# Performance work log

Measured on AMD Instinct MI355X. Metric: run time of the kernel, lower is better.

The kernel has to match this reference:

```python
import jax, jax.numpy as jnp
import numpy as np

N_NODES = 100_000
N_EDGES = 2_500_000
HID = 32
SE3_NORM = 1.0 / np.sqrt(32.0)  # e3nn path normalization for 32x0e -> 32x0e


def setup_inputs() -> dict:
    key = jax.random.key(0)
    ks = jax.random.split(key, 14)
    inp = {
        "pos": jax.random.normal(ks[0], (N_NODES, 3), dtype=jnp.float32),
        "edge_index": jax.random.randint(ks[1], (2, N_EDGES), 0, N_NODES, dtype=jnp.int64),
        "Wl1": jax.random.normal(ks[2], (2, HID), dtype=jnp.float32) * 0.5,
        "bl1": jax.random.normal(ks[3], (HID,), dtype=jnp.float32) * 0.1,
        "Wr1": jax.random.normal(ks[4], (2, HID), dtype=jnp.float32) * 0.5,
        "Wl2": jax.random.normal(ks[5], (HID, HID), dtype=jnp.float32) * 0.15,
        "bl2": jax.random.normal(ks[6], (HID,), dtype=jnp.float32) * 0.1,
        "Wr2": jax.random.normal(ks[7], (HID, HID), dtype=jnp.float32) * 0.15,
        "Wse1": jax.random.normal(ks[8], (HID, HID), dtype=jnp.float32) * 0.15,
        "Wse2": jax.random.normal(ks[9], (HID, HID), dtype=jnp.float32) * 0.15,
        "W3": jax.random.normal(ks[10], (HID, HID), dtype=jnp.float32) * 0.15,
        "b3": jax.random.normal(ks[11], (HID,), dtype=jnp.float32) * 0.1,
        "W4": jax.random.normal(ks[12], (HID, 1), dtype=jnp.float32) * 0.15,
        "b4": jax.random.normal(ks[13], (1,), dtype=jnp.float32) * 0.1,
        "alpha": jnp.float32(0.5),
    }
    return inp


def _sage_conv(x, src, dst, Wl, bl, Wr, n_nodes):
    # gather messages from source nodes, scatter-sum onto destination nodes
    agg = jax.ops.segment_sum(x[src], dst, num_segments=n_nodes)  # [N, d_in]
    return agg @ Wl + bl + x @ Wr  # lin_l(agg) + lin_r(x); lin_r has no bias


def reference(pos, edge_index, Wl1, bl1, Wr1, Wl2, bl2, Wr2, Wse1, Wse2, W3, b3, W4, b4, alpha):
    n = pos.shape[0]
    x = pos[:, :2]                       # [N, 2]
    src, dst = edge_index[0], edge_index[1]

    h1 = _sage_conv(x, src, dst, Wl1, bl1, Wr1, n)   # [N, 32]
    h1 = jax.nn.leaky_relu(h1, negative_slope=0.01)  # dropout = identity (eval)
    h1 = (h1 @ Wse1) * SE3_NORM                      # SE3Linear 32x0e->32x0e

    h2 = _sage_conv(h1, src, dst, Wl2, bl2, Wr2, n)
    h2 = jax.nn.leaky_relu(h2, negative_slope=0.01)
    h2 = (h2 @ Wse2) * SE3_NORM

    x_skip = alpha * h1 + h2
    x_out = jax.nn.relu(x_skip @ W3 + b3)            # mlp3 (dropout identity)
    pred = x_out @ W4 + b4                           # mlp4
    return pred.squeeze(-1)                          # [N]
```

## Files before the change

### kernel.cpp

```cpp
#include <hip/hip_runtime.h>
#include <hip/hip_fp16.h>

#define HID 32
#define LEAKY 0.01f
#define SE3NORM 0.17677669529663687f
#define SCAN_TILE 1024
#define NBK 128
#define GA 256


__global__ void k_bhist(const int* __restrict__ ei, int* __restrict__ bh,
                        int E, int B1, int chunk) {
    extern __shared__ int lh[];
    int g = blockIdx.x;
    for (int i = threadIdx.x; i < B1; i += 256) lh[i] = 0;
    __syncthreads();
    int beg = g * chunk, end = min(E, beg + chunk);
    for (int e = beg + (int)threadIdx.x; e < end; e += 256)
        atomicAdd(&lh[ei[E + e] >> 7], 1);
    __syncthreads();
    for (int b = threadIdx.x; b < B1; b += 256) bh[b * GA + g] = lh[b];
}

__global__ void k_scan1(int* __restrict__ data, int* __restrict__ bsum, int M) {
    __shared__ int lds[256];
    int t = threadIdx.x;
    int base = blockIdx.x * SCAN_TILE + t * 4;
    int v0 = (base + 0 < M) ? data[base + 0] : 0;
    int v1 = (base + 1 < M) ? data[base + 1] : 0;
    int v2 = (base + 2 < M) ? data[base + 2] : 0;
    int v3 = (base + 3 < M) ? data[base + 3] : 0;
    int s = v0 + v1 + v2 + v3;
    lds[t] = s;
    __syncthreads();
    for (int off = 1; off < 256; off <<= 1) {
        int x = (t >= off) ? lds[t - off] : 0;
        __syncthreads();
        lds[t] += x;
        __syncthreads();
    }
    int ex = lds[t] - s;
    if (base + 0 < M) data[base + 0] = ex;
    if (base + 1 < M) data[base + 1] = ex + v0;
    if (base + 2 < M) data[base + 2] = ex + v0 + v1;
    if (base + 3 < M) data[base + 3] = ex + v0 + v1 + v2;
    if (t == 255) bsum[blockIdx.x] = lds[255];
}

__global__ void k_scan2(int* __restrict__ bsum, int B) {
    __shared__ int lds[256];
    int t = threadIdx.x;
    int v = (t < B) ? bsum[t] : 0;
    lds[t] = v;
    __syncthreads();
    for (int off = 1; off < 256; off <<= 1) {
        int x = (t >= off) ? lds[t - off] : 0;
        __syncthreads();
        lds[t] += x;
        __syncthreads();
    }
    if (t < B) bsum[t] = lds[t] - v;
}

__global__ void k_scan3(int* __restrict__ data, const int* __restrict__ bsum,
                        int* __restrict__ cursor, int M, int N) {
    int i = blockIdx.x * blockDim.x + threadIdx.x;
    if (i >= M) return;
    int off = data[i] + bsum[i / SCAN_TILE];
    data[i] = off;
    if (cursor && i < N) cursor[i] = off;
}

__global__ void k_bscatter(const int* __restrict__ ei, const int* __restrict__ bh,
                           int* __restrict__ bucketed, int E, int B1, int chunk) {
    extern __shared__ int cur[];
    int g = blockIdx.x;
    for (int b = threadIdx.x; b < B1; b += 256) cur[b] = bh[b * GA + g];
    __syncthreads();
    int beg = g * chunk, end = min(E, beg + chunk);
    for (int e = beg + (int)threadIdx.x; e < end; e += 256) {
        int d = ei[E + e];
        int s = ei[e];
        int b = d >> 7;
        int p = atomicAdd(&cur[b], 1);
        bucketed[p] = s | ((d & (NBK - 1)) << 24);
    }
}

__global__ void k_bsort(const int* __restrict__ bh, const int* __restrict__ bucketed,
                        int* __restrict__ sorted_src, int* __restrict__ offsets,
                        int E, int N, int B1) {
    __shared__ int hist[NBK], sc[NBK], base[NBK];
    int b = blockIdx.x;
    int t = threadIdx.x;
    int bs = bh[b * GA];
    int be = (b == B1 - 1) ? E : bh[(b + 1) * GA];
    if (t < NBK) hist[t] = 0;
    __syncthreads();
    for (int e = bs + t; e < be; e += 256)
        atomicAdd(&hist[bucketed[e] >> 24], 1);
    __syncthreads();
    int v = (t < NBK) ? hist[t] : 0;
    if (t < NBK) sc[t] = v;
    __syncthreads();
    for (int off = 1; off < NBK; off <<= 1) {
        int x = (t < NBK && t >= off) ? sc[t - off] : 0;
        __syncthreads();
        if (t < NBK) sc[t] += x;
        __syncthreads();
    }
    if (t < NBK) base[t] = sc[t] - v;
    __syncthreads();
    if (t < NBK) hist[t] = base[t];
    __syncthreads();
    for (int e = bs + t; e < be; e += 256) {
        int pv = bucketed[e];
        int p = atomicAdd(&hist[pv >> 24], 1);
        sorted_src[bs + p] = pv & 0x00FFFFFF;
    }
    int node = b * NBK + t;
    if (t < NBK && node < N) offsets[node] = bs + base[t];
    if (b == B1 - 1 && t == 0) offsets[N] = E;
}

__global__ void k_hist_rank(const int* __restrict__ ei, int* __restrict__ hist,
                            int* __restrict__ rank, int E) {
    int base = (blockIdx.x * blockDim.x + threadIdx.x) * 4;
#pragma unroll
    for (int u = 0; u < 4; u++) {
        int e = base + u;
        if (e < E) rank[e] = atomicAdd(&hist[ei[E + e]], 1);
    }
}
__global__ void k_hist(const int* __restrict__ ei, int* __restrict__ hist, int E) {
    int base = (blockIdx.x * blockDim.x + threadIdx.x) * 4;
#pragma unroll
    for (int u = 0; u < 4; u++) {
        int e = base + u;
        if (e < E) atomicAdd(&hist[ei[E + e]], 1);
    }
}
__global__ void k_scatter_rank(const int* __restrict__ ei, const int* __restrict__ offsets,
                               const int* __restrict__ rank, int* __restrict__ sorted_src, int E) {
    int base = (blockIdx.x * blockDim.x + threadIdx.x) * 4;
#pragma unroll
    for (int u = 0; u < 4; u++) {
        int e = base + u;
        if (e < E) sorted_src[offsets[ei[E + e]] + rank[e]] = ei[e];
    }
}
__global__ void k_scatter_atomic(const int* __restrict__ ei, int* __restrict__ cursor,
                                 int* __restrict__ sorted_src, int E) {
    int base = (blockIdx.x * blockDim.x + threadIdx.x) * 4;
#pragma unroll
    for (int u = 0; u < 4; u++) {
        int e = base + u;
        if (e < E) {
            int p = atomicAdd(&cursor[ei[E + e]], 1);
            sorted_src[p] = ei[e];
        }
    }
}

__global__ void k_node1(const int* __restrict__ offsets, const int* __restrict__ sorted_src,
                        const float* __restrict__ pos,
                        const float* __restrict__ Wl1, const float* __restrict__ bl1,
                        const float* __restrict__ Wr1, const float* __restrict__ Wse1,
                        __half* __restrict__ h1out, int N) {
    __shared__ float sWl1[2 * HID], sWr1[2 * HID], sbl1[HID], sWse1[HID * HID];
    for (int i = threadIdx.x; i < 2 * HID; i += blockDim.x) { sWl1[i] = Wl1[i]; sWr1[i] = Wr1[i]; }
    for (int i = threadIdx.x; i < HID; i += blockDim.x) sbl1[i] = bl1[i];
    for (int i = threadIdx.x; i < HID * HID; i += blockDim.x) sWse1[i] = Wse1[i];
    __syncthreads();
    int i = blockIdx.x * blockDim.x + threadIdx.x;
    if (i >= N) return;
    int beg = offsets[i], end = offsets[i + 1];
    float a0 = 0.f, a1 = 0.f;
    int e = beg;
    for (; e + 4 <= end; e += 4) {
        int s0 = sorted_src[e], s1 = sorted_src[e + 1], s2 = sorted_src[e + 2], s3 = sorted_src[e + 3];
        a0 += pos[s0 * 3] + pos[s1 * 3] + pos[s2 * 3] + pos[s3 * 3];
        a1 += pos[s0 * 3 + 1] + pos[s1 * 3 + 1] + pos[s2 * 3 + 1] + pos[s3 * 3 + 1];
    }
    for (; e < end; e++) {
        int s = sorted_src[e];
        a0 += pos[s * 3];
        a1 += pos[s * 3 + 1];
    }
    float x0 = pos[3 * i], x1 = pos[3 * i + 1];
    float h[HID];
#pragma unroll
    for (int j = 0; j < HID; j++) {
        float v = a0 * sWl1[j] + a1 * sWl1[HID + j] + sbl1[j] + x0 * sWr1[j] + x1 * sWr1[HID + j];
        h[j] = v > 0.f ? v : LEAKY * v;
    }
    union Pack8 { __half h[8]; float4 v; };
#pragma unroll
    for (int c = 0; c < HID / 8; c++) {
        Pack8 p;
#pragma unroll
        for (int jj = 0; jj < 8; jj++) {
            int j = c * 8 + jj;
            float acc = 0.f;
#pragma unroll
            for (int k = 0; k < HID; k++) acc += h[k] * sWse1[k * HID + j];
            p.h[jj] = __float2half(acc * SE3NORM);
        }
        *(float4*)&h1out[(size_t)i * HID + c * 8] = p.v;
    }
}

__global__ void k_node2out(const int* __restrict__ offsets, const int* __restrict__ sorted_src,
                           const __half* __restrict__ h1,
                           const float* __restrict__ Wl2, const float* __restrict__ bl2,
                           const float* __restrict__ Wr2, const float* __restrict__ Wse2,
                           const float* __restrict__ W3, const float* __restrict__ b3,
                           const float* __restrict__ W4, const float* __restrict__ b4,
                           const float* __restrict__ alpha_p,
                           float* __restrict__ out, int N) {
    __shared__ float sWl2[HID * HID], sWr2[HID * HID], sWse2[HID * HID], sW3[HID * HID];
    __shared__ float sbl2[HID], sb3[HID], sW4[HID];
    __shared__ float sb4, salpha;
    __shared__ float sA[32][HID + 1], sB[32][HID + 1];
    for (int i = threadIdx.x; i < HID * HID; i += blockDim.x) {
        sWl2[i] = Wl2[i]; sWr2[i] = Wr2[i]; sWse2[i] = Wse2[i]; sW3[i] = W3[i];
    }
    for (int i = threadIdx.x; i < HID; i += blockDim.x) { sbl2[i] = bl2[i]; sb3[i] = b3[i]; sW4[i] = W4[i]; }
    if (threadIdx.x == 0) { sb4 = b4[0]; salpha = alpha_p[0]; }
    __syncthreads();

    const int lt = threadIdx.x;
    const int nodeL = lt >> 3;
    const int t = lt & 7;
    const int node = blockIdx.x * 32 + nodeL;
    const bool live = node < N;

    float hvr[4];
    if (live) {
        int beg = offsets[node], end = offsets[node + 1];
        float4 acc = make_float4(0.f, 0.f, 0.f, 0.f);
        int e = beg;
        for (; e + 4 <= end; e += 4) {
            int s0 = sorted_src[e], s1 = sorted_src[e + 1];
            int s2 = sorted_src[e + 2], s3 = sorted_src[e + 3];
            float2 r0 = *(const float2*)&h1[(size_t)s0 * HID + t * 4];
            float2 r1 = *(const float2*)&h1[(size_t)s1 * HID + t * 4];
            float2 r2 = *(const float2*)&h1[(size_t)s2 * HID + t * 4];
            float2 r3 = *(const float2*)&h1[(size_t)s3 * HID + t * 4];
            const float2* rs[4] = {&r0, &r1, &r2, &r3};
#pragma unroll
            for (int u = 0; u < 4; u++) {
                __half2 p01 = *(const __half2*)&rs[u]->x;
                __half2 p23 = *(const __half2*)&rs[u]->y;
                acc.x += __low2float(p01); acc.y += __high2float(p01);
                acc.z += __low2float(p23); acc.w += __high2float(p23);
            }
        }
        for (; e < end; e++) {
            int s = sorted_src[e];
            float2 r = *(const float2*)&h1[(size_t)s * HID + t * 4];
            __half2 p01 = *(const __half2*)&r.x;
            __half2 p23 = *(const __half2*)&r.y;
            acc.x += __low2float(p01); acc.y += __high2float(p01);
            acc.z += __low2float(p23); acc.w += __high2float(p23);
        }
        float2 ro = *(const float2*)&h1[(size_t)node * HID + t * 4];
        __half2 o01 = *(const __half2*)&ro.x;
        __half2 o23 = *(const __half2*)&ro.y;
        hvr[0] = __low2float(o01); hvr[1] = __high2float(o01);
        hvr[2] = __low2float(o23); hvr[3] = __high2float(o23);
        sA[nodeL][t * 4 + 0] = acc.x; sA[nodeL][t * 4 + 1] = acc.y;
        sA[nodeL][t * 4 + 2] = acc.z; sA[nodeL][t * 4 + 3] = acc.w;
        sB[nodeL][t * 4 + 0] = hvr[0]; sB[nodeL][t * 4 + 1] = hvr[1];
        sB[nodeL][t * 4 + 2] = hvr[2]; sB[nodeL][t * 4 + 3] = hvr[3];
    }
    __syncthreads();

    float h2r[4];
    if (live) {
#pragma unroll
        for (int jj = 0; jj < 4; jj++) {
            int j = t * 4 + jj;
            float acc = sbl2[j];
#pragma unroll
            for (int k = 0; k < HID; k++)
                acc += sA[nodeL][k] * sWl2[k * HID + j] + sB[nodeL][k] * sWr2[k * HID + j];
            h2r[jj] = acc > 0.f ? acc : LEAKY * acc;
        }
    }
    __syncthreads();
    if (live) {
#pragma unroll
        for (int jj = 0; jj < 4; jj++) sA[nodeL][t * 4 + jj] = h2r[jj];
    }
    __syncthreads();

    if (live) {
#pragma unroll
        for (int jj = 0; jj < 4; jj++) {
            int j = t * 4 + jj;
            float acc = 0.f;
#pragma unroll
            for (int k = 0; k < HID; k++) acc += sA[nodeL][k] * sWse2[k * HID + j];
            sB[nodeL][j] = salpha * hvr[jj] + acc * SE3NORM;
        }
    }
    __syncthreads();

    float part = 0.f;
#pragma unroll
    for (int jj = 0; jj < 4; jj++) {
        int j = t * 4 + jj;
        float acc = sb3[j];
        if (live) {
#pragma unroll
            for (int k = 0; k < HID; k++) acc += sB[nodeL][k] * sW3[k * HID + j];
        }
        part += (acc > 0.f ? acc : 0.f) * sW4[j];
    }
    part += __shfl_xor(part, 1);
    part += __shfl_xor(part, 2);
    part += __shfl_xor(part, 4);
    if (live && t == 0) out[node] = part + sb4;
}

extern "C" void kernel_launch(void* const* d_in, const int* in_sizes, int n_in,
                              void* d_out, int out_size, void* d_ws, size_t ws_size,
                              hipStream_t stream) {
    const float* pos  = (const float*)d_in[0];
    const int*   ei   = (const int*)d_in[1];
    const float* Wl1  = (const float*)d_in[2];
    const float* bl1  = (const float*)d_in[3];
    const float* Wr1  = (const float*)d_in[4];
    const float* Wl2  = (const float*)d_in[5];
    const float* bl2  = (const float*)d_in[6];
    const float* Wr2  = (const float*)d_in[7];
    const float* Wse1 = (const float*)d_in[8];
    const float* Wse2 = (const float*)d_in[9];
    const float* W3   = (const float*)d_in[10];
    const float* b3   = (const float*)d_in[11];
    const float* W4   = (const float*)d_in[12];
    const float* b4   = (const float*)d_in[13];
    const float* alp  = (const float*)d_in[14];
    float* out = (float*)d_out;

    const int N = in_sizes[0] / 3;
    const int E = in_sizes[1] / 2;
    const int blk = 256;
    const size_t h1bytes = (size_t)N * HID * sizeof(__half);

    const int B1 = (N + NBK - 1) / NBK;
    const int M2 = B1 * GA;
    const int S2 = (M2 + SCAN_TILE - 1) / SCAN_TILE;
    {
        int* bh         = (int*)d_ws;
        int* bsum       = bh + M2;
        int* bucketed   = bsum + 256;
        int* sorted_src = bucketed + E;
        int* offsets    = sorted_src + E;
        uintptr_t hp = ((uintptr_t)(offsets + N + 1) + 15) & ~(uintptr_t)15;
        size_t need = (hp - (uintptr_t)d_ws) + h1bytes;
        if (need <= ws_size && S2 <= 256) {
            __half* h1 = (__half*)hp;
            const int chunk = (E + GA - 1) / GA;
            const size_t ldsB = (size_t)B1 * sizeof(int);
            k_bhist<<<GA, 256, ldsB, stream>>>(ei, bh, E, B1, chunk);
            k_scan1<<<S2, 256, 0, stream>>>(bh, bsum, M2);
            k_scan2<<<1, 256, 0, stream>>>(bsum, S2);
            k_scan3<<<(M2 + blk - 1) / blk, blk, 0, stream>>>(bh, bsum, nullptr, M2, 0);
            k_bscatter<<<GA, 256, ldsB, stream>>>(ei, bh, bucketed, E, B1, chunk);
            k_bsort<<<B1, 256, 0, stream>>>(bh, bucketed, sorted_src, offsets, E, N, B1);
            k_node1<<<(N + blk - 1) / blk, blk, 0, stream>>>(offsets, sorted_src, pos,
                                                             Wl1, bl1, Wr1, Wse1, h1, N);
            k_node2out<<<(N + 31) / 32, 256, 0, stream>>>(offsets, sorted_src, h1,
                                                          Wl2, bl2, Wr2, Wse2,
                                                          W3, b3, W4, b4, alp, out, N);
            return;
        }
    }

    const int M = N + 1;
    const int B = (M + SCAN_TILE - 1) / SCAN_TILE;
    int* hist       = (int*)d_ws;
    int* offsets    = hist + M;
    int* bsum       = offsets + M;
    int* sorted_src = bsum + 256;
    int* aux        = sorted_src + E;
    uintptr_t hpA = ((uintptr_t)(aux + E) + 15) & ~(uintptr_t)15;
    uintptr_t hpB = ((uintptr_t)(aux + N) + 15) & ~(uintptr_t)15;
    size_t needA = (hpA - (uintptr_t)d_ws) + h1bytes;
    const bool useRank = (needA <= ws_size);
    __half* h1 = (__half*)(useRank ? hpA : hpB);

    hipMemsetAsync(hist, 0, (size_t)M * sizeof(int), stream);
    const int egrid4 = (E / 4 + blk) / blk;
    if (useRank) {
        k_hist_rank<<<egrid4, blk, 0, stream>>>(ei, hist, aux, E);
    } else {
        k_hist<<<egrid4, blk, 0, stream>>>(ei, hist, E);
    }
    k_scan1<<<B, 256, 0, stream>>>(hist, bsum, M);
    k_scan2<<<1, 256, 0, stream>>>(bsum, B);
    k_scan3<<<(M + blk - 1) / blk, blk, 0, stream>>>(hist, bsum, useRank ? nullptr : aux, M, N);
    int* offs = hist;
    if (useRank) {
        k_scatter_rank<<<egrid4, blk, 0, stream>>>(ei, offs, aux, sorted_src, E);
    } else {
        k_scatter_atomic<<<egrid4, blk, 0, stream>>>(ei, aux, sorted_src, E);
    }
    k_node1<<<(N + blk - 1) / blk, blk, 0, stream>>>(offs, sorted_src, pos, Wl1, bl1, Wr1, Wse1, h1, N);
    k_node2out<<<(N + 31) / 32, 256, 0, stream>>>(offs, sorted_src, h1, Wl2, bl2, Wr2, Wse2,
                                                  W3, b3, W4, b4, alp, out, N);
}
```

Baseline: 288.8 us.

## Partition edges by source range to localize layer-2 gathers in cache

Edges are bucketed by source-node range (4 ranges) as well as destination block. Layer-2 aggregation then runs as four passes, each gathering h1 rows from only a quarter of the nodes so the working set fits in cache, and accumulates into an fp32 agg2 buffer. A separate head kernel does the dense MLP afterwards. The price is extra passes over agg2 (read-modify-write on each pass), more bucket bins and scan work, and extra kernel launches. GA is also halved and the fallback path is simplified.

```diff
diff --git a/kernel.cpp b/kernel.cpp
--- a/kernel.cpp
+++ b/kernel.cpp
@@ -6,20 +6,29 @@
 #define SE3NORM 0.17677669529663687f
 #define SCAN_TILE 1024
 #define NBK 128
-#define GA 256
-
+#define GA 128
+#define RR 4
+
+
+__device__ __forceinline__ int src_range(int s, unsigned magic) {
+    int r = (int)__umulhi((unsigned)s, magic);
+    return r < RR - 1 ? r : RR - 1;
+}
 
 __global__ void k_bhist(const int* __restrict__ ei, int* __restrict__ bh,
-                        int E, int B1, int chunk) {
+                        int E, int B1, int B2, int chunk, unsigned magic) {
     extern __shared__ int lh[];
     int g = blockIdx.x;
-    for (int i = threadIdx.x; i < B1; i += 256) lh[i] = 0;
+    for (int i = threadIdx.x; i < B2; i += 256) lh[i] = 0;
     __syncthreads();
     int beg = g * chunk, end = min(E, beg + chunk);
-    for (int e = beg + (int)threadIdx.x; e < end; e += 256)
-        atomicAdd(&lh[ei[E + e] >> 7], 1);
-    __syncthreads();
-    for (int b = threadIdx.x; b < B1; b += 256) bh[b * GA + g] = lh[b];
+    for (int e = beg + (int)threadIdx.x; e < end; e += 256) {
+        int s = ei[e];
+        int d = ei[E + e];
+        atomicAdd(&lh[src_range(s, magic) * B1 + (d >> 7)], 1);
+    }
+    __syncthreads();
+    for (int b = threadIdx.x; b < B2; b += 256) bh[b * GA + g] = lh[b];
 }
 
 __global__ void k_scan1(int* __restrict__ data, int* __restrict__ bsum, int M) {
@@ -50,8 +59,13 @@
 __global__ void k_scan2(int* __restrict__ bsum, int B) {
     __shared__ int lds[256];
     int t = threadIdx.x;
-    int v = (t < B) ? bsum[t] : 0;
-    lds[t] = v;
+    int base = t * 4;
+    int v0 = (base + 0 < B) ? bsum[base + 0] : 0;
+    int v1 = (base + 1 < B) ? bsum[base + 1] : 0;
+    int v2 = (base + 2 < B) ? bsum[base + 2] : 0;
+    int v3 = (base + 3 < B) ? bsum[base + 3] : 0;
+    int s = v0 + v1 + v2 + v3;
+    lds[t] = s;
     __syncthreads();
     for (int off = 1; off < 256; off <<= 1) {
         int x = (t >= off) ? lds[t - off] : 0;
@@ -59,7 +73,11 @@
         lds[t] += x;
         __syncthreads();
     }
-    if (t < B) bsum[t] = lds[t] - v;
+    int ex = lds[t] - s;
+    if (base + 0 < B) bsum[base + 0] = ex;
+    if (base + 1 < B) bsum[base + 1] = ex + v0;
+    if (base + 2 < B) bsum[base + 2] = ex + v0 + v1;
+    if (base + 3 < B) bsum[base + 3] = ex + v0 + v1 + v2;
 }
 
 __global__ void k_scan3(int* __restrict__ data, const int* __restrict__ bsum,
@@ -72,16 +90,17 @@
 }
 
 __global__ void k_bscatter(const int* __restrict__ ei, const int* __restrict__ bh,
-                           int* __restrict__ bucketed, int E, int B1, int chunk) {
+                           int* __restrict__ bucketed, int E, int B1, int B2,
+                           int chunk, unsigned magic) {
     extern __shared__ int cur[];
     int g = blockIdx.x;
-    for (int b = threadIdx.x; b < B1; b += 256) cur[b] = bh[b * GA + g];
+    for (int b = threadIdx.x; b < B2; b += 256) cur[b] = bh[b * GA + g];
     __syncthreads();
     int beg = g * chunk, end = min(E, beg + chunk);
     for (int e = beg + (int)threadIdx.x; e < end; e += 256) {
+        int s = ei[e];
         int d = ei[E + e];
-        int s = ei[e];
-        int b = d >> 7;
+        int b = src_range(s, magic) * B1 + (d >> 7);
         int p = atomicAdd(&cur[b], 1);
         bucketed[p] = s | ((d & (NBK - 1)) << 24);
     }
@@ -89,12 +108,14 @@
 
 __global__ void k_bsort(const int* __restrict__ bh, const int* __restrict__ bucketed,
                         int* __restrict__ sorted_src, int* __restrict__ offsets,
-                        int E, int N, int B1) {
+                        int E, int N, int B1, int B2) {
     __shared__ int hist[NBK], sc[NBK], base[NBK];
-    int b = blockIdx.x;
+    int b2 = blockIdx.x;
+    int r  = b2 / B1;
+    int cb = b2 - r * B1;
     int t = threadIdx.x;
-    int bs = bh[b * GA];
-    int be = (b == B1 - 1) ? E : bh[(b + 1) * GA];
+    int bs = bh[b2 * GA];
+    int be = (b2 == B2 - 1) ? E : bh[(b2 + 1) * GA];
     if (t < NBK) hist[t] = 0;
     __syncthreads();
     for (int e = bs + t; e < be; e += 256)
@@ -118,9 +139,9 @@
         int p = atomicAdd(&hist[pv >> 24], 1);
         sorted_src[bs + p] = pv & 0x00FFFFFF;
     }
-    int node = b * NBK + t;
-    if (t < NBK && node < N) offsets[node] = bs + base[t];
-    if (b == B1 - 1 && t == 0) offsets[N] = E;
+    int node = cb * NBK + t;
+    if (t < NBK && node < N) offsets[(size_t)r * N + node] = bs + base[t];
+    if (b2 == B2 - 1 && t == 0) offsets[(size_t)RR * N] = E;
 }
 
 __global__ void k_hist_rank(const int* __restrict__ ei, int* __restrict__ hist,
@@ -132,14 +153,6 @@
         if (e < E) rank[e] = atomicAdd(&hist[ei[E + e]], 1);
     }
 }
-__global__ void k_hist(const int* __restrict__ ei, int* __restrict__ hist, int E) {
-    int base = (blockIdx.x * blockDim.x + threadIdx.x) * 4;
-#pragma unroll
-    for (int u = 0; u < 4; u++) {
-        int e = base + u;
-        if (e < E) atomicAdd(&hist[ei[E + e]], 1);
-    }
-}
 __global__ void k_scatter_rank(const int* __restrict__ ei, const int* __restrict__ offsets,
                                const int* __restrict__ rank, int* __restrict__ sorted_src, int E) {
     int base = (blockIdx.x * blockDim.x + threadIdx.x) * 4;
@@ -147,18 +160,6 @@
     for (int u = 0; u < 4; u++) {
         int e = base + u;
         if (e < E) sorted_src[offsets[ei[E + e]] + rank[e]] = ei[e];
-    }
-}
-__global__ void k_scatter_atomic(const int* __restrict__ ei, int* __restrict__ cursor,
-                                 int* __restrict__ sorted_src, int E) {
-    int base = (blockIdx.x * blockDim.x + threadIdx.x) * 4;
-#pragma unroll
-    for (int u = 0; u < 4; u++) {
-        int e = base + u;
-        if (e < E) {
-            int p = atomicAdd(&cursor[ei[E + e]], 1);
-            sorted_src[p] = ei[e];
-        }
     }
 }
 
@@ -166,7 +167,7 @@
                         const float* __restrict__ pos,
                         const float* __restrict__ Wl1, const float* __restrict__ bl1,
                         const float* __restrict__ Wr1, const float* __restrict__ Wse1,
-                        __half* __restrict__ h1out, int N) {
+                        __half* __restrict__ h1out, int N, int Rr) {
     __shared__ float sWl1[2 * HID], sWr1[2 * HID], sbl1[HID], sWse1[HID * HID];
     for (int i = threadIdx.x; i < 2 * HID; i += blockDim.x) { sWl1[i] = Wl1[i]; sWr1[i] = Wr1[i]; }
     for (int i = threadIdx.x; i < HID; i += blockDim.x) sbl1[i] = bl1[i];
@@ -174,18 +175,20 @@
     __syncthreads();
     int i = blockIdx.x * blockDim.x + threadIdx.x;
     if (i >= N) return;
-    int beg = offsets[i], end = offsets[i + 1];
     float a0 = 0.f, a1 = 0.f;
-    int e = beg;
-    for (; e + 4 <= end; e += 4) {
-        int s0 = sorted_src[e], s1 = sorted_src[e + 1], s2 = sorted_src[e + 2], s3 = sorted_src[e + 3];
-        a0 += pos[s0 * 3] + pos[s1 * 3] + pos[s2 * 3] + pos[s3 * 3];
-        a1 += pos[s0 * 3 + 1] + pos[s1 * 3 + 1] + pos[s2 * 3 + 1] + pos[s3 * 3 + 1];
-    }
-    for (; e < end; e++) {
-        int s = sorted_src[e];
-        a0 += pos[s * 3];
-        a1 += pos[s * 3 + 1];
+    for (int r = 0; r < Rr; r++) {
+        int beg = offsets[(size_t)r * N + i], end = offsets[(size_t)r * N + i + 1];
+        int e = beg;
+        for (; e + 4 <= end; e += 4) {
+            int s0 = sorted_src[e], s1 = sorted_src[e + 1], s2 = sorted_src[e + 2], s3 = sorted_src[e + 3];
+            a0 += pos[s0 * 3] + pos[s1 * 3] + pos[s2 * 3] + pos[s3 * 3];
+            a1 += pos[s0 * 3 + 1] + pos[s1 * 3 + 1] + pos[s2 * 3 + 1] + pos[s3 * 3 + 1];
+        }
+        for (; e < end; e++) {
+            int s = sorted_src[e];
+            a0 += pos[s * 3];
+            a1 += pos[s * 3 + 1];
+        }
     }
     float x0 = pos[3 * i], x1 = pos[3 * i + 1];
     float h[HID];
@@ -208,6 +211,132 @@
         }
         *(float4*)&h1out[(size_t)i * HID + c * 8] = p.v;
     }
+}
+
+__global__ void k_node2agg(const int* __restrict__ offsets, const int* __restrict__ sorted_src,
+                           const __half* __restrict__ h1, float* __restrict__ agg2,
+                           int N, int r) {
+    int lt = blockIdx.x * blockDim.x + threadIdx.x;
+    int node = lt >> 3;
+    int t = lt & 7;
+    if (node >= N) return;
+    int beg = offsets[(size_t)r * N + node], end = offsets[(size_t)r * N + node + 1];
+    float4 acc;
+    if (r == 0) acc = make_float4(0.f, 0.f, 0.f, 0.f);
+    else        acc = *(const float4*)&agg2[(size_t)node * HID + t * 4];
+    int e = beg;
+    for (; e + 4 <= end; e += 4) {
+        int s0 = sorted_src[e], s1 = sorted_src[e + 1];
+        int s2 = sorted_src[e + 2], s3 = sorted_src[e + 3];
+        float2 r0 = *(const float2*)&h1[(size_t)s0 * HID + t * 4];
+        float2 r1 = *(const float2*)&h1[(size_t)s1 * HID + t * 4];
+        float2 r2 = *(const float2*)&h1[(size_t)s2 * HID + t * 4];
+        float2 r3 = *(const float2*)&h1[(size_t)s3 * HID + t * 4];
+        const float2* rs[4] = {&r0, &r1, &r2, &r3};
+#pragma unroll
+        for (int u = 0; u < 4; u++) {
+            __half2 p01 = *(const __half2*)&rs[u]->x;
+            __half2 p23 = *(const __half2*)&rs[u]->y;
+            acc.x += __low2float(p01); acc.y += __high2float(p01);
+            acc.z += __low2float(p23); acc.w += __high2float(p23);
+        }
+    }
+    for (; e < end; e++) {
+        int s = sorted_src[e];
+        float2 rr = *(const float2*)&h1[(size_t)s * HID + t * 4];
+        __half2 p01 = *(const __half2*)&rr.x;
+        __half2 p23 = *(const __half2*)&rr.y;
+        acc.x += __low2float(p01); acc.y += __high2float(p01);
+        acc.z += __low2float(p23); acc.w += __high2float(p23);
+    }
+    *(float4*)&agg2[(size_t)node * HID + t * 4] = acc;
+}
+
+__global__ void k_node2head(const float* __restrict__ agg2, const __half* __restrict__ h1,
+                            const float* __restrict__ Wl2, const float* __restrict__ bl2,
+                            const float* __restrict__ Wr2, const float* __restrict__ Wse2,
+                            const float* __restrict__ W3, const float* __restrict__ b3,
+                            const float* __restrict__ W4, const float* __restrict__ b4,
+                            const float* __restrict__ alpha_p,
+                            float* __restrict__ out, int N) {
+    __shared__ float sWl2[HID * HID], sWr2[HID * HID], sWse2[HID * HID], sW3[HID * HID];
+    __shared__ float sbl2[HID], sb3[HID], sW4[HID];
+    __shared__ float sb4, salpha;
+    __shared__ float sA[32][HID + 1], sB[32][HID + 1];
+    for (int i = threadIdx.x; i < HID * HID; i += blockDim.x) {
+        sWl2[i] = Wl2[i]; sWr2[i] = Wr2[i]; sWse2[i] = Wse2[i]; sW3[i] = W3[i];
+    }
+    for (int i = threadIdx.x; i < HID; i += blockDim.x) { sbl2[i] = bl2[i]; sb3[i] = b3[i]; sW4[i] = W4[i]; }
+    if (threadIdx.x == 0) { sb4 = b4[0]; salpha = alpha_p[0]; }
+    __syncthreads();
+
+    const int lt = threadIdx.x;
+    const int nodeL = lt >> 3;
+    const int t = lt & 7;
+    const int node = blockIdx.x * 32 + nodeL;
+    const bool live = node < N;
+
+    float hvr[4];
+    if (live) {
+        float4 a = *(const float4*)&agg2[(size_t)node * HID + t * 4];
+        float2 ro = *(const float2*)&h1[(size_t)node * HID + t * 4];
+        __half2 o01 = *(const __half2*)&ro.x;
+        __half2 o23 = *(const __half2*)&ro.y;
+        hvr[0] = __low2float(o01); hvr[1] = __high2float(o01);
+        hvr[2] = __low2float(o23); hvr[3] = __high2float(o23);
+        sA[nodeL][t * 4 + 0] = a.x; sA[nodeL][t * 4 + 1] = a.y;
+        sA[nodeL][t * 4 + 2] = a.z; sA[nodeL][t * 4 + 3] = a.w;
+        sB[nodeL][t * 4 + 0] = hvr[0]; sB[nodeL][t * 4 + 1] = hvr[1];
+        sB[nodeL][t * 4 + 2] = hvr[2]; sB[nodeL][t * 4 + 3] = hvr[3];
+    }
+    __syncthreads();
+
+    float h2r[4];
+    if (live) {
+#pragma unroll
+        for (int jj = 0; jj < 4; jj++) {
+            int j = t * 4 + jj;
+            float acc = sbl2[j];
+#pragma unroll
+            for (int k = 0; k < HID; k++)
+                acc += sA[nodeL][k] * sWl2[k * HID + j] + sB[nodeL][k] * sWr2[k * HID + j];
+            h2r[jj] = acc > 0.f ? acc : LEAKY * acc;
+        }
+    }
+    __syncthreads();
+    if (live) {
+#pragma unroll
+        for (int jj = 0; jj < 4; jj++) sA[nodeL][t * 4 + jj] = h2r[jj];
+    }
+    __syncthreads();
+
+    if (live) {
+#pragma unroll
+        for (int jj = 0; jj < 4; jj++) {
+            int j = t * 4 + jj;
+            float acc = 0.f;
+#pragma unroll
+            for (int k = 0; k < HID; k++) acc += sA[nodeL][k] * sWse2[k * HID + j];
+            sB[nodeL][j] = salpha * hvr[jj] + acc * SE3NORM;
+        }
+    }
+    __syncthreads();
+
+    float part = 0.f;
+#pragma unroll
+    for (int jj = 0; jj < 4; jj++) {
+        int j = t * 4 + jj;
+        float acc = sb3[j];
+        if (live) {
+#pragma unroll
+            for (int k = 0; k < HID; k++) acc += sB[nodeL][k] * sW3[k * HID + j];
+        }
+        part += (acc > 0.f ? acc : 0.f) * sW4[j];
+    }
+    part += __shfl_xor(part, 1);
+    part += __shfl_xor(part, 2);
+    part += __shfl_xor(part, 4);
+    if (live && t == 0) out[node] = part + sb4;
 }
 
 __global__ void k_node2out(const int* __restrict__ offsets, const int* __restrict__ sorted_src,
@@ -228,39 +357,20 @@
     for (int i = threadIdx.x; i < HID; i += blockDim.x) { sbl2[i] = bl2[i]; sb3[i] = b3[i]; sW4[i] = W4[i]; }
     if (threadIdx.x == 0) { sb4 = b4[0]; salpha = alpha_p[0]; }
     __syncthreads();
-
     const int lt = threadIdx.x;
     const int nodeL = lt >> 3;
     const int t = lt & 7;
     const int node = blockIdx.x * 32 + nodeL;
     const bool live = node < N;
-
     float hvr[4];
     if (live) {
         int beg = offsets[node], end = offsets[node + 1];
         float4 acc = make_float4(0.f, 0.f, 0.f, 0.f);
-        int e = beg;
-        for (; e + 4 <= end; e += 4) {
-            int s0 = sorted_src[e], s1 = sorted_src[e + 1];
-            int s2 = sorted_src[e + 2], s3 = sorted_src[e + 3];
-            float2 r0 = *(const float2*)&h1[(size_t)s0 * HID + t * 4];
-            float2 r1 = *(const float2*)&h1[(size_t)s1 * HID + t * 4];
-            float2 r2 = *(const float2*)&h1[(size_t)s2 * HID + t * 4];
-            float2 r3 = *(const float2*)&h1[(size_t)s3 * HID + t * 4];
-            const float2* rs[4] = {&r0, &r1, &r2, &r3};
-#pragma unroll
-            for (int u = 0; u < 4; u++) {
-                __half2 p01 = *(const __half2*)&rs[u]->x;
-                __half2 p23 = *(const __half2*)&rs[u]->y;
-                acc.x += __low2float(p01); acc.y += __high2float(p01);
-                acc.z += __low2float(p23); acc.w += __high2float(p23);
-            }
-        }
-        for (; e < end; e++) {
+        for (int e = beg; e < end; e++) {
             int s = sorted_src[e];
-            float2 r = *(const float2*)&h1[(size_t)s * HID + t * 4];
-            __half2 p01 = *(const __half2*)&r.x;
-            __half2 p23 = *(const __half2*)&r.y;
+            float2 rr = *(const float2*)&h1[(size_t)s * HID + t * 4];
+            __half2 p01 = *(const __half2*)&rr.x;
+            __half2 p23 = *(const __half2*)&rr.y;
             acc.x += __low2float(p01); acc.y += __high2float(p01);
             acc.z += __low2float(p23); acc.w += __high2float(p23);
         }
@@ -275,7 +385,6 @@
         sB[nodeL][t * 4 + 2] = hvr[2]; sB[nodeL][t * 4 + 3] = hvr[3];
     }
     __syncthreads();
-
     float h2r[4];
     if (live) {
 #pragma unroll
@@ -294,7 +403,6 @@
         for (int jj = 0; jj < 4; jj++) sA[nodeL][t * 4 + jj] = h2r[jj];
     }
     __syncthreads();
-
     if (live) {
 #pragma unroll
         for (int jj = 0; jj < 4; jj++) {
@@ -306,7 +414,6 @@
         }
     }
     __syncthreads();
-
     float part = 0.f;
 #pragma unroll
     for (int jj = 0; jj < 4; jj++) {
@@ -350,31 +457,39 @@
     const size_t h1bytes = (size_t)N * HID * sizeof(__half);
 
     const int B1 = (N + NBK - 1) / NBK;
-    const int M2 = B1 * GA;
+    const int B2 = RR * B1;
+    const int M2 = B2 * GA;
     const int S2 = (M2 + SCAN_TILE - 1) / SCAN_TILE;
+    const int rangeSize = (N + RR - 1) / RR;
+    const unsigned magic = (unsigned)(((1ULL << 32) + rangeSize - 1) / rangeSize);
     {
         int* bh         = (int*)d_ws;
         int* bsum       = bh + M2;
-        int* bucketed   = bsum + 256;
-        int* sorted_src = bucketed + E;
+        int* region     = bsum + 1024;
+        size_t regionInts = (size_t)E > (size_t)N * HID ? (size_t)E : (size_t)N * HID;
+        int* sorted_src = region + regionInts;
         int* offsets    = sorted_src + E;
-        uintptr_t hp = ((uintptr_t)(offsets + N + 1) + 15) & ~(uintptr_t)15;
+        uintptr_t hp = ((uintptr_t)(offsets + (size_t)RR * N + 1) + 15) & ~(uintptr_t)15;
         size_t need = (hp - (uintptr_t)d_ws) + h1bytes;
-        if (need <= ws_size && S2 <= 256) {
+        if (need <= ws_size && S2 <= 1024) {
+            int* bucketed = region;
+            float* agg2   = (float*)region;
             __half* h1 = (__half*)hp;
             const int chunk = (E + GA - 1) / GA;
-            const size_t ldsB = (size_t)B1 * sizeof(int);
-            k_bhist<<<GA, 256, ldsB, stream>>>(ei, bh, E, B1, chunk);
+            const size_t ldsB = (size_t)B2 * sizeof(int);
+            k_bhist<<<GA, 256, ldsB, stream>>>(ei, bh, E, B1, B2, chunk, magic);
             k_scan1<<<S2, 256, 0, stream>>>(bh, bsum, M2);
             k_scan2<<<1, 256, 0, stream>>>(bsum, S2);
             k_scan3<<<(M2 + blk - 1) / blk, blk, 0, stream>>>(bh, bsum, nullptr, M2, 0);
-            k_bscatter<<<GA, 256, ldsB, stream>>>(ei, bh, bucketed, E, B1, chunk);
-            k_bsort<<<B1, 256, 0, stream>>>(bh, bucketed, sorted_src, offsets, E, N, B1);
+            k_bscatter<<<GA, 256, ldsB, stream>>>(ei, bh, bucketed, E, B1, B2, chunk, magic);
+            k_bsort<<<B2, 256, 0, stream>>>(bh, bucketed, sorted_src, offsets, E, N, B1, B2);
             k_node1<<<(N + blk - 1) / blk, blk, 0, stream>>>(offsets, sorted_src, pos,
-                                                             Wl1, bl1, Wr1, Wse1, h1, N);
-            k_node2out<<<(N + 31) / 32, 256, 0, stream>>>(offsets, sorted_src, h1,
-                                                          Wl2, bl2, Wr2, Wse2,
-                                                          W3, b3, W4, b4, alp, out, N);
+                                                             Wl1, bl1, Wr1, Wse1, h1, N, RR);
+            const int agrid = ((N * 8) + blk - 1) / blk;
+            for (int r = 0; r < RR; r++)
+                k_node2agg<<<agrid, blk, 0, stream>>>(offsets, sorted_src, h1, agg2, N, r);
+            k_node2head<<<(N + 31) / 32, 256, 0, stream>>>(agg2, h1, Wl2, bl2, Wr2, Wse2,
+                                                           W3, b3, W4, b4, alp, out, N);
             return;
         }
     }
@@ -382,33 +497,21 @@
     const int M = N + 1;
     const int B = (M + SCAN_TILE - 1) / SCAN_TILE;
     int* hist       = (int*)d_ws;
-    int* offsets    = hist + M;
-    int* bsum       = offsets + M;
-    int* sorted_src = bsum + 256;
+    int* bsum       = hist + M;
+    int* sorted_src = bsum + 1024;
     int* aux        = sorted_src + E;
     uintptr_t hpA = ((uintptr_t)(aux + E) + 15) & ~(uintptr_t)15;
-    uintptr_t hpB = ((uintptr_t)(aux + N) + 15) & ~(uintptr_t)15;
-    size_t needA = (hpA - (uintptr_t)d_ws) + h1bytes;
-    const bool useRank = (needA <= ws_size);
-    __half* h1 = (__half*)(useRank ? hpA : hpB);
+    __half* h1 = (__half*)hpA;
 
     hipMemsetAsync(hist, 0, (size_t)M * sizeof(int), stream);
     const int egrid4 = (E / 4 + blk) / blk;
-    if (useRank) {
-        k_hist_rank<<<egrid4, blk, 0, stream>>>(ei, hist, aux, E);
-    } else {
-        k_hist<<<egrid4, blk, 0, stream>>>(ei, hist, E);
-    }
+    k_hist_rank<<<egrid4, blk, 0, stream>>>(ei, hist, aux, E);
     k_scan1<<<B, 256, 0, stream>>>(hist, bsum, M);
     k_scan2<<<1, 256, 0, stream>>>(bsum, B);
-    k_scan3<<<(M + blk - 1) / blk, blk, 0, stream>>>(hist, bsum, useRank ? nullptr : aux, M, N);
+    k_scan3<<<(M + blk - 1) / blk, blk, 0, stream>>>(hist, bsum, nullptr, M, N);
     int* offs = hist;
-    if (useRank) {
-        k_scatter_rank<<<egrid4, blk, 0, stream>>>(ei, offs, aux, sorted_src, E);
-    } else {
-        k_scatter_atomic<<<egrid4, blk, 0, stream>>>(ei, aux, sorted_src, E);
-    }
-    k_node1<<<(N + blk - 1) / blk, blk, 0, stream>>>(offs, sorted_src, pos, Wl1, bl1, Wr1, Wse1, h1, N);
+    k_scatter_rank<<<egrid4, blk, 0, stream>>>(ei, offs, aux, sorted_src, E);
+    k_node1<<<(N + blk - 1) / blk, blk, 0, stream>>>(offs, sorted_src, pos, Wl1, bl1, Wr1, Wse1, h1, N, 1);
     k_node2out<<<(N + 31) / 32, 256, 0, stream>>>(offs, sorted_src, h1, Wl2, bl2, Wr2, Wse2,
                                                   W3, b3, W4, b4, alp, out, N);
 }
```

Measured after the change: 333.9 us. 15.6% more time.

## Split layer-2 gather into two source-half passes for better h1 cache locality

Applied to the files above, without the earlier changes.

The bucket sort now splits each destination's edges into two sub-bins by whether the source index falls in the lower or upper half of nodes, and emits a doubled offset array. Layer-2 aggregation runs as two passes: one sums the lower-half sources into an fp32 scratch buffer, then the fused head kernel adds the upper-half sources and finishes the MLP. Each pass gathers from only half of h1, so the working set is meant to fit better in cache. The cost is an extra kernel launch and an N×32 fp32 round-trip through memory. The fallback atomic-sort path is removed, and the scan2 kernel is widened to handle up to 1024 block sums.

```diff
diff --git a/kernel.cpp b/kernel.cpp
--- a/kernel.cpp
+++ b/kernel.cpp
@@ -7,6 +7,8 @@
 #define SCAN_TILE 1024
 #define NBK 128
 #define GA 256
+
+typedef float vf4 __attribute__((ext_vector_type(4)));
 
 
 __global__ void k_bhist(const int* __restrict__ ei, int* __restrict__ bh,
@@ -50,8 +52,13 @@
 __global__ void k_scan2(int* __restrict__ bsum, int B) {
     __shared__ int lds[256];
     int t = threadIdx.x;
-    int v = (t < B) ? bsum[t] : 0;
-    lds[t] = v;
+    int base = t * 4;
+    int v0 = (base + 0 < B) ? bsum[base + 0] : 0;
+    int v1 = (base + 1 < B) ? bsum[base + 1] : 0;
+    int v2 = (base + 2 < B) ? bsum[base + 2] : 0;
+    int v3 = (base + 3 < B) ? bsum[base + 3] : 0;
+    int s = v0 + v1 + v2 + v3;
+    lds[t] = s;
     __syncthreads();
     for (int off = 1; off < 256; off <<= 1) {
         int x = (t >= off) ? lds[t - off] : 0;
@@ -59,16 +66,17 @@
         lds[t] += x;
         __syncthreads();
     }
-    if (t < B) bsum[t] = lds[t] - v;
-}
-
-__global__ void k_scan3(int* __restrict__ data, const int* __restrict__ bsum,
-                        int* __restrict__ cursor, int M, int N) {
+    int ex = lds[t] - s;
+    if (base + 0 < B) bsum[base + 0] = ex;
+    if (base + 1 < B) bsum[base + 1] = ex + v0;
+    if (base + 2 < B) bsum[base + 2] = ex + v0 + v1;
+    if (base + 3 < B) bsum[base + 3] = ex + v0 + v1 + v2;
+}
+
+__global__ void k_scan3(int* __restrict__ data, const int* __restrict__ bsum, int M) {
     int i = blockIdx.x * blockDim.x + threadIdx.x;
     if (i >= M) return;
-    int off = data[i] + bsum[i / SCAN_TILE];
-    data[i] = off;
-    if (cursor && i < N) cursor[i] = off;
+    data[i] += bsum[i / SCAN_TILE];
 }
 
 __global__ void k_bscatter(const int* __restrict__ ei, const int* __restrict__ bh,
@@ -88,81 +96,47 @@
 }
 
 __global__ void k_bsort(const int* __restrict__ bh, const int* __restrict__ bucketed,
-                        int* __restrict__ sorted_src, int* __restrict__ offsets,
-                        int E, int N, int B1) {
-    __shared__ int hist[NBK], sc[NBK], base[NBK];
+                        int* __restrict__ sorted_src, int* __restrict__ off2,
+                        int E, int N, int B1, int half) {
+    __shared__ int hist[256], base[256], lds[256];
     int b = blockIdx.x;
     int t = threadIdx.x;
     int bs = bh[b * GA];
     int be = (b == B1 - 1) ? E : bh[(b + 1) * GA];
-    if (t < NBK) hist[t] = 0;
-    __syncthreads();
-    for (int e = bs + t; e < be; e += 256)
-        atomicAdd(&hist[bucketed[e] >> 24], 1);
-    __syncthreads();
-    int v = (t < NBK) ? hist[t] : 0;
-    if (t < NBK) sc[t] = v;
-    __syncthreads();
-    for (int off = 1; off < NBK; off <<= 1) {
-        int x = (t < NBK && t >= off) ? sc[t - off] : 0;
-        __syncthreads();
-        if (t < NBK) sc[t] += x;
-        __syncthreads();
-    }
-    if (t < NBK) base[t] = sc[t] - v;
-    __syncthreads();
-    if (t < NBK) hist[t] = base[t];
+    hist[t] = 0;
     __syncthreads();
     for (int e = bs + t; e < be; e += 256) {
         int pv = bucketed[e];
-        int p = atomicAdd(&hist[pv >> 24], 1);
+        int bin = ((pv >> 24) << 1) | ((pv & 0x00FFFFFF) >= half);
+        atomicAdd(&hist[bin], 1);
+    }
+    __syncthreads();
+    int v = hist[t];
+    lds[t] = v;
+    __syncthreads();
+    for (int off = 1; off < 256; off <<= 1) {
+        int x = (t >= off) ? lds[t - off] : 0;
+        __syncthreads();
+        lds[t] += x;
+        __syncthreads();
+    }
+    int ex = lds[t] - v;
+    base[t] = ex;
+    __syncthreads();
+    hist[t] = ex;
+    __syncthreads();
+    for (int e = bs + t; e < be; e += 256) {
+        int pv = bucketed[e];
+        int bin = ((pv >> 24) << 1) | ((pv & 0x00FFFFFF) >= half);
+        int p = atomicAdd(&hist[bin], 1);
         sorted_src[bs + p] = pv & 0x00FFFFFF;
     }
-    int node = b * NBK + t;
-    if (t < NBK && node < N) offsets[node] = bs + base[t];
-    if (b == B1 - 1 && t == 0) offsets[N] = E;
-}
-
-__global__ void k_hist_rank(const int* __restrict__ ei, int* __restrict__ hist,
-                            int* __restrict__ rank, int E) {
-    int base = (blockIdx.x * blockDim.x + threadIdx.x) * 4;
-#pragma unroll
-    for (int u = 0; u < 4; u++) {
-        int e = base + u;
-        if (e < E) rank[e] = atomicAdd(&hist[ei[E + e]], 1);
-    }
-}
-__global__ void k_hist(const int* __restrict__ ei, int* __restrict__ hist, int E) {
-    int base = (blockIdx.x * blockDim.x + threadIdx.x) * 4;
-#pragma unroll
-    for (int u = 0; u < 4; u++) {
-        int e = base + u;
-        if (e < E) atomicAdd(&hist[ei[E + e]], 1);
-    }
-}
-__global__ void k_scatter_rank(const int* __restrict__ ei, const int* __restrict__ offsets,
-                               const int* __restrict__ rank, int* __restrict__ sorted_src, int E) {
-    int base = (blockIdx.x * blockDim.x + threadIdx.x) * 4;
-#pragma unroll
-    for (int u = 0; u < 4; u++) {
-        int e = base + u;
-        if (e < E) sorted_src[offsets[ei[E + e]] + rank[e]] = ei[e];
-    }
-}
-__global__ void k_scatter_atomic(const int* __restrict__ ei, int* __restrict__ cursor,
-                                 int* __restrict__ sorted_src, int E) {
-    int base = (blockIdx.x * blockDim.x + threadIdx.x) * 4;
-#pragma unroll
-    for (int u = 0; u < 4; u++) {
-        int e = base + u;
-        if (e < E) {
-            int p = atomicAdd(&cursor[ei[E + e]], 1);
-            sorted_src[p] = ei[e];
-        }
-    }
-}
-
-__global__ void k_node1(const int* __restrict__ offsets, const int* __restrict__ sorted_src,
+    int node = b * NBK + (t >> 1);
+    if (node < N) off2[node * 2 + (t & 1)] = bs + base[t];
+    if (b == B1 - 1 && t == 0) off2[2 * N] = E;
+}
+
+__global__ void k_node1(const int* __restrict__ off2, const int* __restrict__ sorted_src,
                         const float* __restrict__ pos,
                         const float* __restrict__ Wl1, const float* __restrict__ bl1,
                         const float* __restrict__ Wr1, const float* __restrict__ Wse1,
@@ -174,7 +148,7 @@
     __syncthreads();
     int i = blockIdx.x * blockDim.x + threadIdx.x;
     if (i >= N) return;
-    int beg = offsets[i], end = offsets[i + 1];
+    int beg = off2[i * 2], end = off2[i * 2 + 2];
     float a0 = 0.f, a1 = 0.f;
     int e = beg;
     for (; e + 4 <= end; e += 4) {
@@ -210,8 +184,47 @@
     }
 }
 
-__global__ void k_node2out(const int* __restrict__ offsets, const int* __restrict__ sorted_src,
-                           const __half* __restrict__ h1,
+__global__ void k_agg0(const int* __restrict__ off2, const int* __restrict__ sorted_src,
+                       const __half* __restrict__ h1, float* __restrict__ agg2, int N) {
+    int lt = blockIdx.x * blockDim.x + threadIdx.x;
+    int node = lt >> 3;
+    int t = lt & 7;
+    if (node >= N) return;
+    int beg = off2[node * 2], end = off2[node * 2 + 1];
+    float4 acc = make_float4(0.f, 0.f, 0.f, 0.f);
+    int e = beg;
+    for (; e + 4 <= end; e += 4) {
+        int s0 = __builtin_nontemporal_load(&sorted_src[e]);
+        int s1 = __builtin_nontemporal_load(&sorted_src[e + 1]);
+        int s2 = __builtin_nontemporal_load(&sorted_src[e + 2]);
+        int s3 = __builtin_nontemporal_load(&sorted_src[e + 3]);
+        float2 r0 = *(const float2*)&h1[(size_t)s0 * HID + t * 4];
+        float2 r1 = *(const float2*)&h1[(size_t)s1 * HID + t * 4];
+        float2 r2 = *(const float2*)&h1[(size_t)s2 * HID + t * 4];
+        float2 r3 = *(const float2*)&h1[(size_t)s3 * HID + t * 4];
+        const float2* rs[4] = {&r0, &r1, &r2, &r3};
+#pragma unroll
+        for (int u = 0; u < 4; u++) {
+            __half2 p01 = *(const __half2*)&rs[u]->x;
+            __half2 p23 = *(const __half2*)&rs[u]->y;
+            acc.x += __low2float(p01); acc.y += __high2float(p01);
+            acc.z += __low2float(p23); acc.w += __high2float(p23);
+        }
+    }
+    for (; e < end; e++) {
+        int s = __builtin_nontemporal_load(&sorted_src[e]);
+        float2 rr = *(const float2*)&h1[(size_t)s * HID + t * 4];
+        __half2 p01 = *(const __half2*)&rr.x;
+        __half2 p23 = *(const __half2*)&rr.y;
+        acc.x += __low2float(p01); acc.y += __high2float(p01);
+        acc.z += __low2float(p23); acc.w += __high2float(p23);
+    }
+    vf4 av; av.x = acc.x; av.y = acc.y; av.z = acc.z; av.w = acc.w;
+    __builtin_nontemporal_store(av, (vf4*)&agg2[(size_t)node * HID + t * 4]);
+}
+
+__global__ void k_agg1head(const int* __restrict__ off2, const int* __restrict__ sorted_src,
+                           const __half* __restrict__ h1, const float* __restrict__ agg2,
                            const float* __restrict__ Wl2, const float* __restrict__ bl2,
                            const float* __restrict__ Wr2, const float* __restrict__ Wse2,
                            const float* __restrict__ W3, const float* __restrict__ b3,
@@ -237,12 +250,15 @@
 
     float hvr[4];
     if (live) {
-        int beg = offsets[node], end = offsets[node + 1];
-        float4 acc = make_float4(0.f, 0.f, 0.f, 0.f);
+        vf4 p0 = __builtin_nontemporal_load((const vf4*)&agg2[(size_t)node * HID + t * 4]);
+        float4 acc = make_float4(p0.x, p0.y, p0.z, p0.w);
+        int beg = off2[node * 2 + 1], end = off2[node * 2 + 2];
         int e = beg;
         for (; e + 4 <= end; e += 4) {
-            int s0 = sorted_src[e], s1 = sorted_src[e + 1];
-            int s2 = sorted_src[e + 2], s3 = sorted_src[e + 3];
+            int s0 = __builtin_nontemporal_load(&sorted_src[e]);
+            int s1 = __builtin_nontemporal_load(&sorted_src[e + 1]);
+            int s2 = __builtin_nontemporal_load(&sorted_src[e + 2]);
+            int s3 = __builtin_nontemporal_load(&sorted_src[e + 3]);
             float2 r0 = *(const float2*)&h1[(size_t)s0 * HID + t * 4];
             float2 r1 = *(const float2*)&h1[(size_t)s1 * HID + t * 4];
             float2 r2 = *(const float2*)&h1[(size_t)s2 * HID + t * 4];
@@ -257,10 +273,10 @@
             }
         }
         for (; e < end; e++) {
-            int s = sorted_src[e];
-            float2 r = *(const float2*)&h1[(size_t)s * HID + t * 4];
-            __half2 p01 = *(const __half2*)&r.x;
-            __half2 p23 = *(const __half2*)&r.y;
+            int s = __builtin_nontemporal_load(&sorted_src[e]);
+            float2 rr = *(const float2*)&h1[(size_t)s * HID + t * 4];
+            __half2 p01 = *(const __half2*)&rr.x;
+            __half2 p23 = *(const __half2*)&rr.y;
             acc.x += __low2float(p01); acc.y += __high2float(p01);
             acc.z += __low2float(p23); acc.w += __high2float(p23);
         }
@@ -281,11 +297,11 @@
 #pragma unroll
         for (int jj = 0; jj < 4; jj++) {
             int j = t * 4 + jj;
-            float acc = sbl2[j];
+            float a2 = sbl2[j];
 #pragma unroll
             for (int k = 0; k < HID; k++)
-                acc += sA[nodeL][k] * sWl2[k * HID + j] + sB[nodeL][k] * sWr2[k * HID + j];
-            h2r[jj] = acc > 0.f ? acc : LEAKY * acc;
+                a2 += sA[nodeL][k] * sWl2[k * HID + j] + sB[nodeL][k] * sWr2[k * HID + j];
+            h2r[jj] = a2 > 0.f ? a2 : LEAKY * a2;
         }
     }
     __syncthreads();
@@ -294,29 +310,27 @@
         for (int jj = 0; jj < 4; jj++) sA[nodeL][t * 4 + jj] = h2r[jj];
     }
     __syncthreads();
-
     if (live) {
 #pragma unroll
         for (int jj = 0; jj < 4; jj++) {
             int j = t * 4 + jj;
-            float acc = 0.f;
-#pragma unroll
-            for (int k = 0; k < HID; k++) acc += sA[nodeL][k] * sWse2[k * HID + j];
-            sB[nodeL][j] = salpha * hvr[jj] + acc * SE3NORM;
-        }
-    }
-    __syncthreads();
-
+            float a2 = 0.f;
+#pragma unroll
+            for (int k = 0; k < HID; k++) a2 += sA[nodeL][k] * sWse2[k * HID + j];
+            sB[nodeL][j] = salpha * hvr[jj] + a2 * SE3NORM;
+        }
+    }
+    __syncthreads();
     float part = 0.f;
 #pragma unroll
     for (int jj = 0; jj < 4; jj++) {
         int j = t * 4 + jj;
-        float acc = sb3[j];
+        float a2 = sb3[j];
         if (live) {
 #pragma unroll
-            for (int k = 0; k < HID; k++) acc += sB[nodeL][k] * sW3[k * HID + j];
-        }
-        part += (acc > 0.f ? acc : 0.f) * sW4[j];
+            for (int k = 0; k < HID; k++) a2 += sB[nodeL][k] * sW3[k * HID + j];
+        }
+        part += (a2 > 0.f ? a2 : 0.f) * sW4[j];
     }
     part += __shfl_xor(part, 1);
     part += __shfl_xor(part, 2);
@@ -347,68 +361,37 @@
     const int N = in_sizes[0] / 3;
     const int E = in_sizes[1] / 2;
     const int blk = 256;
-    const size_t h1bytes = (size_t)N * HID * sizeof(__half);
-
+    const int half = (N + 1) / 2;
     const int B1 = (N + NBK - 1) / NBK;
     const int M2 = B1 * GA;
     const int S2 = (M2 + SCAN_TILE - 1) / SCAN_TILE;
-    {
-        int* bh         = (int*)d_ws;
-        int* bsum       = bh + M2;
-        int* bucketed   = bsum + 256;
-        int* sorted_src = bucketed + E;
-        int* offsets    = sorted_src + E;
-        uintptr_t hp = ((uintptr_t)(offsets + N + 1) + 15) & ~(uintptr_t)15;
-        size_t need = (hp - (uintptr_t)d_ws) + h1bytes;
-        if (need <= ws_size && S2 <= 256) {
-            __half* h1 = (__half*)hp;
-            const int chunk = (E + GA - 1) / GA;
-            const size_t ldsB = (size_t)B1 * sizeof(int);
-            k_bhist<<<GA, 256, ldsB, stream>>>(ei, bh, E, B1, chunk);
-            k_scan1<<<S2, 256, 0, stream>>>(bh, bsum, M2);
-            k_scan2<<<1, 256, 0, stream>>>(bsum, S2);
-            k_scan3<<<(M2 + blk - 1) / blk, blk, 0, stream>>>(bh, bsum, nullptr, M2, 0);
-            k_bscatter<<<GA, 256, ldsB, stream>>>(ei, bh, bucketed, E, B1, chunk);
-            k_bsort<<<B1, 256, 0, stream>>>(bh, bucketed, sorted_src, offsets, E, N, B1);
-            k_node1<<<(N + blk - 1) / blk, blk, 0, stream>>>(offsets, sorted_src, pos,
-                                                             Wl1, bl1, Wr1, Wse1, h1, N);
-            k_node2out<<<(N + 31) / 32, 256, 0, stream>>>(offsets, sorted_src, h1,
-                                                          Wl2, bl2, Wr2, Wse2,
-                                                          W3, b3, W4, b4, alp, out, N);
-            return;
-        }
-    }
-
-    const int M = N + 1;
-    const int B = (M + SCAN_TILE - 1) / SCAN_TILE;
-    int* hist       = (int*)d_ws;
-    int* offsets    = hist + M;
-    int* bsum       = offsets + M;
-    int* sorted_src = bsum + 256;
-    int* aux        = sorted_src + E;
-    uintptr_t hpA = ((uintptr_t)(aux + E) + 15) & ~(uintptr_t)15;
-    uintptr_t hpB = ((uintptr_t)(aux + N) + 15) & ~(uintptr_t)15;
-    size_t needA = (hpA - (uintptr_t)d_ws) + h1bytes;
-    const bool useRank = (needA <= ws_size);
-    __half* h1 = (__half*)(useRank ? hpA : hpB);
-
-    hipMemsetAsync(hist, 0, (size_t)M * sizeof(int), stream);
-    const int egrid4 = (E / 4 + blk) / blk;
-    if (useRank) {
-        k_hist_rank<<<egrid4, blk, 0, stream>>>(ei, hist, aux, E);
-    } else {
-        k_hist<<<egrid4, blk, 0, stream>>>(ei, hist, E);
-    }
-    k_scan1<<<B, 256, 0, stream>>>(hist, bsum, M);
-    k_scan2<<<1, 256, 0, stream>>>(bsum, B);
-    k_scan3<<<(M + blk - 1) / blk, blk, 0, stream>>>(hist, bsum, useRank ? nullptr : aux, M, N);
-    int* offs = hist;
-    if (useRank) {
-        k_scatter_rank<<<egrid4, blk, 0, stream>>>(ei, offs, aux, sorted_src, E);
-    } else {
-        k_scatter_atomic<<<egrid4, blk, 0, stream>>>(ei, aux, sorted_src, E);
-    }
-    k_node1<<<(N + blk - 1) / blk, blk, 0, stream>>>(offs, sorted_src, pos, Wl1, bl1, Wr1, Wse1, h1, N);
-    k_node2out<<<(N + 31) / 32, 256, 0, stream>>>(offs, sorted_src, h1, Wl2, bl2, Wr2, Wse2,
+
+    int* bh         = (int*)d_ws;
+    int* bsum       = bh + M2;
+    int* region     = bsum + 1024;
+    size_t regionInts = (size_t)E > (size_t)N * HID ? (size_t)E : (size_t)N * HID;
+    int* sorted_src = region + regionInts;
+    int* off2       = sorted_src + E;
+    uintptr_t hp = ((uintptr_t)(off2 + (size_t)2 * N + 1) + 15) & ~(uintptr_t)15;
+    size_t need = (hp - (uintptr_t)d_ws) + (size_t)N * HID * sizeof(__half);
+    if (need > ws_size || S2 > 1024) return;
+    int* bucketed = region;
+    float* agg2   = (float*)region;
+    __half* h1    = (__half*)hp;
+
+    const int chunk = (E + GA - 1) / GA;
+    const size_t ldsB = (size_t)B1 * sizeof(int);
+    k_bhist<<<GA, 256, ldsB, stream>>>(ei, bh, E, B1, chunk);
+    k_scan1<<<S2, 256, 0, stream>>>(bh, bsum, M2);
+    k_scan2<<<1, 256, 0, stream>>>(bsum, S2);
+    k_scan3<<<(M2 + blk - 1) / blk, blk, 0, stream>>>(bh, bsum, M2);
+    k_bscatter<<<GA, 256, ldsB, stream>>>(ei, bh, bucketed, E, B1, chunk);
+    k_bsort<<<B1, 256, 0, stream>>>(bh, bucketed, sorted_src, off2, E, N, B1, half);
+    k_node1<<<(N + blk - 1) / blk, blk, 0, stream>>>(off2, sorted_src, pos,
+                                                     Wl1, bl1, Wr1, Wse1, h1, N);
+    const int agrid = ((N * 8) + blk - 1) / blk;
+    k_agg0<<<agrid, blk, 0, stream>>>(off2, sorted_src, h1, agg2, N);
+    k_agg1head<<<(N + 31) / 32, 256, 0, stream>>>(off2, sorted_src, h1, agg2,
+                                                  Wl2, bl2, Wr2, Wse2,
                                                   W3, b3, W4, b4, alp, out, N);
 }
```

Result: slower. 315.4 us (+9.2%).
